# Kernel tuning notes

Measured on AMD Instinct MI355X. Metric: run time of the kernel, lower is better.

## Reference

```python
import jax, jax.numpy as jnp
import numpy as np

B, N = 4, 65536
NUM_GROUP, GROUP_SIZE = 512, 64
EMB = 60


def setup_inputs() -> dict:
    key = jax.random.key(0)
    ks = jax.random.split(key, 8)
    inp = {
        'xyz': jax.random.uniform(ks[0], (B, N, 3), jnp.float32),
        'color': jax.random.uniform(ks[1], (B, N, 3), jnp.float32),
        'W1': jax.random.normal(ks[2], (6, 64), jnp.float32) * 0.2,
        'b1': jnp.zeros((64,), jnp.float32),
        'W2': jax.random.normal(ks[3], (64, 128), jnp.float32) * 0.1,
        'b2': jnp.zeros((128,), jnp.float32),
        'W3': jax.random.normal(ks[4], (128, 256), jnp.float32) * 0.08,
        'b3': jnp.zeros((256,), jnp.float32),
        'W4': jax.random.normal(ks[5], (256, 512), jnp.float32) * 0.06,
        'b4': jnp.zeros((512,), jnp.float32),
        'Wp': jax.random.normal(ks[6], (512, EMB), jnp.float32) * 0.04,
        'bp': jnp.zeros((EMB,), jnp.float32),
    }
    return inp


def fps(xyz, n):
    """Farthest point sampling. xyz: (B,N,3) -> centers (B,n,3)."""
    b, npts, _ = xyz.shape
    start = jnp.zeros((b,), jnp.int32)
    d0 = jnp.full((b, npts), 1e10, xyz.dtype)

    def step(carry, _):
        dists, last = carry
        p = jnp.take_along_axis(xyz, last[:, None, None], axis=1)  # (B,1,3)
        d = jnp.sum((xyz - p) ** 2, axis=-1)                       # (B,N)
        dists = jnp.minimum(dists, d)
        nxt = jnp.argmax(dists, axis=-1).astype(jnp.int32)
        return (dists, nxt), nxt

    (_, _), rest = jax.lax.scan(step, (d0, start), None, length=n - 1)
    idx = jnp.concatenate([start[:, None], rest.T], axis=1)        # (B,n)
    return jax.vmap(lambda pts, i: pts[i])(xyz, idx)


def knn_idx(k, xyz, new_xyz):
    """Indices of k nearest points in xyz for each query in new_xyz.
    xyz: (B,N,3), new_xyz: (B,S,3) -> (B,S,k) int32. Matches
    square_distance + topk(largest=False)."""
    sq = (jnp.sum(new_xyz ** 2, -1)[..., None]
          + jnp.sum(xyz ** 2, -1)[:, None, :]
          - 2.0 * jnp.einsum('bsc,bnc->bsn', new_xyz, xyz))        # (B,S,N)
    _, idx = jax.lax.top_k(-sq, k)
    return idx


def reference(xyz, color, W1, b1, W2, b2, W3, b3, W4, b4, Wp, bp):
    # --- Group: FPS centers + KNN neighborhood gather + centering ---
    center = fps(xyz, NUM_GROUP)                                   # (B,G,3)
    idx = knn_idx(GROUP_SIZE, xyz, center)                         # (B,G,M)
    gather = jax.vmap(lambda pts, i: pts[i])                       # pts[(B,)N,3], i (G,M)
    neighborhood = gather(xyz, idx) - center[:, :, None, :]        # (B,G,M,3) centered
    neighborhood_color = gather(color, idx)                        # (B,G,M,3)
    feats = jnp.concatenate([neighborhood, neighborhood_color], -1)  # (B,G,M,6)

    # --- PointNet: per-point MLP -> max over group -> projection ---
    x = jax.nn.relu(feats @ W1 + b1)
    x = jax.nn.relu(x @ W2 + b2)
    x = jax.nn.relu(x @ W3 + b3)
    x = jax.nn.relu(x @ W4 + b4)                                   # (B,G,M,512)
    x = jnp.max(x, axis=2)                                         # (B,G,512)
    emb = x @ Wp + bp                                              # (B,G,60)
    return emb, center
```

## Files before the change

### kernel.cpp

```cpp
#include <hip/hip_runtime.h>
#include <stdint.h>

#define DI __device__ __forceinline__

typedef _Float16 f16x8 __attribute__((ext_vector_type(8)));
typedef float f32x4 __attribute__((ext_vector_type(4)));

constexpr int kB = 4;
constexpr int kN = 65536;
constexpr int kG = 512;
constexpr int kM = 64;
constexpr int kE = 60;
constexpr int GRD = 20;
constexpr int NCELL = GRD * GRD * GRD;
constexpr float CW = 1.0f / 20.0f;

constexpr int FPS_SUB = 8;
constexpr int FPS_PT_T = kN / FPS_SUB / 1024;

constexpr size_t OFF_WIN    = 0;
constexpr size_t OFF_CNT    = OFF_WIN + (size_t)kB * kG * 8;
constexpr size_t OFF_CCNT   = OFF_CNT + (size_t)kB * kG * 4;
constexpr size_t ZERO_BYTES = OFF_CCNT + (size_t)kB * NCELL * 4;
constexpr size_t OFF_CSTART = ZERO_BYTES;
constexpr size_t OFF_CUR    = OFF_CSTART + (size_t)kB * (NCELL + 1) * 4;
constexpr size_t OFF_SW1    = ((OFF_CUR + (size_t)kB * NCELL * 4) + 255) & ~(size_t)255;
constexpr size_t OFF_SW2    = OFF_SW1 + 2048 * 2;
constexpr size_t OFF_SW3    = OFF_SW2 + 8192 * 2;
constexpr size_t OFF_SW4    = OFF_SW3 + 32768 * 2;
constexpr size_t OFF_WPT    = OFF_SW4 + 131072 * 2;
constexpr size_t OFF_SORT   = ((OFF_WPT + 60 * 512 * 4) + 255) & ~(size_t)255;
constexpr size_t OFF_KIDX   = OFF_SORT + (size_t)kB * kN * 16;

DI int cellof(float x) {
  int c = (int)(x * (float)GRD);
  return min(GRD - 1, max(0, c));
}
DI unsigned orderable(float f) {
  unsigned u = __float_as_uint(f);
  return (u & 0x80000000u) ? ~u : (u | 0x80000000u);
}

__global__ void k_zero(uint32_t* p, int nwords) {
  int i = blockIdx.x * blockDim.x + threadIdx.x;
  int st = gridDim.x * blockDim.x;
  for (; i < nwords; i += st) p[i] = 0u;
}

DI void swz(const float* __restrict__ W, _Float16* __restrict__ sw,
            int total, int nks, int Kreal, int N, int i0, int st) {
  for (int i = i0; i < total; i += st) {
    int j = i & 7, lane = (i >> 3) & 63, rest = i >> 9;
    int ks = rest % nks, nt = rest / nks;
    int k = ks * 32 + ((lane >> 4) << 3) + j;
    int n = nt * 16 + (lane & 15);
    sw[i] = (_Float16)((k < Kreal) ? W[k * N + n] : 0.f);
  }
}

__global__ void k_prep(const float* __restrict__ W1, const float* __restrict__ W2,
                       const float* __restrict__ W3, const float* __restrict__ W4,
                       const float* __restrict__ Wp,
                       _Float16* __restrict__ sw1, _Float16* __restrict__ sw2,
                       _Float16* __restrict__ sw3, _Float16* __restrict__ sw4,
                       float* __restrict__ wpt) {
  int i0 = blockIdx.x * blockDim.x + threadIdx.x;
  int st = gridDim.x * blockDim.x;
  swz(W1, sw1, 2048, 1, 6, 64, i0, st);
  swz(W2, sw2, 8192, 2, 64, 128, i0, st);
  swz(W3, sw3, 32768, 4, 128, 256, i0, st);
  swz(W4, sw4, 131072, 8, 256, 512, i0, st);
  for (int i = i0; i < 60 * 512; i += st) { int n = i >> 9, k = i & 511; wpt[i] = Wp[k * 60 + n]; }
}

__global__ __launch_bounds__(1024) void k_fps(const float* __restrict__ xyz,
                                              float* __restrict__ outC,
                                              unsigned long long* __restrict__ win,
                                              unsigned int* __restrict__ cnt) {
  const int b = blockIdx.x >> 3, sub = blockIdx.x & 7;
  const int tid = threadIdx.x;
  const float* X = xyz + (size_t)b * kN * 3;
  float px[FPS_PT_T], py[FPS_PT_T], pz[FPS_PT_T], dd[FPS_PT_T];
#pragma unroll
  for (int j = 0; j < FPS_PT_T; ++j) {
    int p = sub * (kN / FPS_SUB) + j * 1024 + tid;
    px[j] = X[3 * p]; py[j] = X[3 * p + 1]; pz[j] = X[3 * p + 2];
    dd[j] = 1e10f;
  }
  float lx = X[0], ly = X[1], lz = X[2];
  if (sub == 0 && tid == 0) {
    outC[(size_t)b * kG * 3 + 0] = lx;
    outC[(size_t)b * kG * 3 + 1] = ly;
    outC[(size_t)b * kG * 3 + 2] = lz;
  }
  __shared__ unsigned long long wres[16];
  __shared__ float sp[3];
  unsigned long long* winB = win + (size_t)b * kG;
  unsigned int* cntB = cnt + (size_t)b * kG;

  for (int it = 1; it < kG; ++it) {
    unsigned long long best = 0ull;
#pragma unroll
    for (int j = 0; j < FPS_PT_T; ++j) {
      float dx = __fsub_rn(px[j], lx);
      float dy = __fsub_rn(py[j], ly);
      float dz = __fsub_rn(pz[j], lz);
      float d = __fadd_rn(__fadd_rn(__fmul_rn(dx, dx), __fmul_rn(dy, dy)), __fmul_rn(dz, dz));
      float nd = fminf(dd[j], d);
      dd[j] = nd;
      int p = sub * (kN / FPS_SUB) + j * 1024 + tid;
      unsigned long long pk =
          ((unsigned long long)__float_as_uint(nd) << 32) | (unsigned)(0xFFFFFFFFu - (unsigned)p);
      best = (pk > best) ? pk : best;
    }
#pragma unroll
    for (int off = 32; off; off >>= 1) {
      unsigned long long o = __shfl_down(best, (unsigned)off);
      best = (o > best) ? o : best;
    }
    if ((tid & 63) == 0) wres[tid >> 6] = best;
    __syncthreads();
    if (tid == 0) {
      unsigned long long bb = wres[0];
#pragma unroll
      for (int i = 1; i < 16; ++i) bb = (wres[i] > bb) ? wres[i] : bb;
      atomicMax(winB + it, bb | (1ull << 63));
      __threadfence();
      atomicAdd(cntB + it, 1u);
      long bail = 0;
      while (__hip_atomic_load(cntB + it, __ATOMIC_ACQUIRE, __HIP_MEMORY_SCOPE_AGENT) < (unsigned)FPS_SUB) {
        __builtin_amdgcn_s_sleep(1);
        if (++bail > 100000000L) break;
      }
      unsigned long long w = __hip_atomic_load(winB + it, __ATOMIC_ACQUIRE, __HIP_MEMORY_SCOPE_AGENT);
      int wi = (int)(0xFFFFFFFFu - (unsigned)(w & 0xFFFFFFFFu));
      float wx = X[3 * wi], wy = X[3 * wi + 1], wz = X[3 * wi + 2];
      sp[0] = wx; sp[1] = wy; sp[2] = wz;
      if (sub == 0) {
        outC[((size_t)b * kG + it) * 3 + 0] = wx;
        outC[((size_t)b * kG + it) * 3 + 1] = wy;
        outC[((size_t)b * kG + it) * 3 + 2] = wz;
      }
    }
    __syncthreads();
    lx = sp[0]; ly = sp[1]; lz = sp[2];
  }
}

__global__ void k_cellcount(const float* __restrict__ xyz, uint32_t* __restrict__ ccnt) {
  int i = blockIdx.x * blockDim.x + threadIdx.x;
  int st = gridDim.x * blockDim.x;
  for (; i < kB * kN; i += st) {
    int b = i >> 16, p = i & (kN - 1);
    const float* q = xyz + ((size_t)b * kN + p) * 3;
    int cid = (cellof(q[2]) * GRD + cellof(q[1])) * GRD + cellof(q[0]);
    atomicAdd(&ccnt[b * NCELL + cid], 1u);
  }
}

__global__ void k_scan(const uint32_t* __restrict__ ccnt, uint32_t* __restrict__ cstart,
                       uint32_t* __restrict__ cur) {
  int b = blockIdx.x, tid = threadIdx.x;
  const uint32_t* cc = ccnt + (size_t)b * NCELL;
  uint32_t* cs = cstart + (size_t)b * (NCELL + 1);
  uint32_t* cu = cur + (size_t)b * NCELL;
  __shared__ uint32_t part[256];
  const int chunk = 32;
  int c0 = tid * chunk;
  uint32_t s = 0;
  for (int i = 0; i < chunk; ++i) { int c = c0 + i; if (c < NCELL) s += cc[c]; }
  part[tid] = s;
  __syncthreads();
  for (int off = 1; off < 256; off <<= 1) {
    uint32_t add = (tid >= off) ? part[tid - off] : 0u;
    __syncthreads();
    part[tid] += add;
    __syncthreads();
  }
  uint32_t run = part[tid] - s;
  for (int i = 0; i < chunk; ++i) {
    int c = c0 + i;
    if (c < NCELL) { cs[c] = run; cu[c] = run; run += cc[c]; }
  }
  if (tid == 255) cs[NCELL] = run;
}

__global__ void k_scatter(const float* __restrict__ xyz, uint32_t* __restrict__ cur,
                          float4* __restrict__ sorted) {
  int i = blockIdx.x * blockDim.x + threadIdx.x;
  int st = gridDim.x * blockDim.x;
  for (; i < kB * kN; i += st) {
    int b = i >> 16, p = i & (kN - 1);
    const float* q = xyz + ((size_t)b * kN + p) * 3;
    float x = q[0], y = q[1], z = q[2];
    int cid = (cellof(z) * GRD + cellof(y)) * GRD + cellof(x);
    uint32_t pos = atomicAdd(&cur[b * NCELL + cid], 1u);
    sorted[(size_t)b * kN + pos] = make_float4(x, y, z, __uint_as_float((unsigned)p));
  }
}

constexpr int CAP = 8192;

DI void bitonic(unsigned long long* a, int n, int tid) {
  for (int k = 2; k <= n; k <<= 1)
    for (int j = k >> 1; j > 0; j >>= 1) {
      __syncthreads();
      for (int i = tid; i < n; i += 256) {
        int ix = i ^ j;
        if (ix > i) {
          unsigned long long x = a[i], y = a[ix];
          bool up = ((i & k) == 0);
          if ((x > y) == up) { a[i] = y; a[ix] = x; }
        }
      }
    }
  __syncthreads();
}

__global__ __launch_bounds__(256) void k_knn(const float4* __restrict__ sorted,
                                             const uint32_t* __restrict__ cstart,
                                             const float* __restrict__ outC,
                                             uint32_t* __restrict__ kidx) {
  const int bi = blockIdx.x;
  const int b = (bi & 7) >> 1;
  const int g = ((bi >> 3) << 1) | (bi & 1);
  const int tid = threadIdx.x;
  __shared__ unsigned long long cand[CAP];
  __shared__ int nC;
  const float cx = outC[((size_t)b * kG + g) * 3 + 0];
  const float cy = outC[((size_t)b * kG + g) * 3 + 1];
  const float cz = outC[((size_t)b * kG + g) * 3 + 2];
  const float nc = __fadd_rn(__fadd_rn(__fmul_rn(cx, cx), __fmul_rn(cy, cy)), __fmul_rn(cz, cz));
  const float4* SP = sorted + (size_t)b * kN;
  const uint32_t* CS = cstart + (size_t)b * (NCELL + 1);
  const int ccx = cellof(cx), ccy = cellof(cy), ccz = cellof(cz);
  if (tid == 0) nC = 0;
  __syncthreads();
  int plox = 1, phix = 0, ploy = 1, phiy = 0, ploz = 1, phiz = 0;
  for (int r = 1; r <= GRD; ++r) {
    int lox = max(0, ccx - r), hix = min(GRD - 1, ccx + r);
    int loy = max(0, ccy - r), hiy = min(GRD - 1, ccy + r);
    int loz = max(0, ccz - r), hiz = min(GRD - 1, ccz + r);
    for (int z = loz; z <= hiz; ++z)
      for (int y = loy; y <= hiy; ++y) {
        bool rowPrev = (r > 1) && (z >= ploz && z <= phiz && y >= ploy && y <= phiy);
        for (int s = 0; s < 2; ++s) {
          int xa, xb;
          if (!rowPrev) { if (s) break; xa = lox; xb = hix; }
          else if (s == 0) { xa = lox; xb = plox - 1; }
          else { xa = phix + 1; xb = hix; }
          if (xa > xb) continue;
          int c0 = (z * GRD + y) * GRD + xa;
          int i0 = CS[c0];
          int i1 = CS[(z * GRD + y) * GRD + xb + 1];
          for (int i = i0 + tid; i < i1; i += 256) {
            float4 pt = SP[i];
            float npn = __fadd_rn(__fadd_rn(__fmul_rn(pt.x, pt.x), __fmul_rn(pt.y, pt.y)),
                                  __fmul_rn(pt.z, pt.z));
            float dot = __fadd_rn(__fadd_rn(__fmul_rn(cx, pt.x), __fmul_rn(cy, pt.y)),
                                  __fmul_rn(cz, pt.z));
            float sq = __fsub_rn(__fadd_rn(nc, npn), __fmul_rn(2.0f, dot));
            unsigned key = orderable(sq);
            int pos = atomicAdd(&nC, 1);
            if (pos < CAP)
              cand[pos] = ((unsigned long long)key << 32) | (unsigned)__float_as_uint(pt.w);
          }
        }
      }
    __syncthreads();
    int n = min(nC, CAP);
    float rc = 1e30f;
    if (lox > 0) rc = fminf(rc, cx - (float)lox * CW);
    if (hix < GRD - 1) rc = fminf(rc, (float)(hix + 1) * CW - cx);
    if (loy > 0) rc = fminf(rc, cy - (float)loy * CW);
    if (hiy < GRD - 1) rc = fminf(rc, (float)(hiy + 1) * CW - cy);
    if (loz > 0) rc = fminf(rc, cz - (float)loz * CW);
    if (hiz < GRD - 1) rc = fminf(rc, (float)(hiz + 1) * CW - cz);
    float r2 = (rc >= 1e29f) ? 3.0e38f : rc * rc * (1.0f - 1e-5f);
    unsigned keyR = orderable(r2);
    bool done = false;
    if (n >= kM) {
      int np2 = 1;
      while (np2 < n) np2 <<= 1;
      for (int i = n + tid; i < np2; i += 256) cand[i] = ~0ull;
      bitonic(cand, np2, tid);
      unsigned k63 = (unsigned)(cand[kM - 1] >> 32);
      done = (k63 <= keyR);
      if (tid == 0) nC = n;
    }
    __syncthreads();
    if (done) break;
    plox = lox; phix = hix; ploy = loy; phiy = hiy; ploz = loz; phiz = hiz;
  }
  if (tid < kM)
    kidx[((size_t)b * kG + g) * kM + tid] = (uint32_t)(cand[tid] & 0xFFFFFFFFu);
}


template <int Kdim, int Ndim, int SIN, int SOUT>
DI void mfma_layer(const _Float16* __restrict__ Xin, _Float16* __restrict__ Xout,
                   const _Float16* __restrict__ Wsw, const float* __restrict__ bias,
                   int wave, int lane) {
  constexpr int NKS = Kdim / 32;
  constexpr int NTW = Ndim / 64;
  constexpr int CH = (NTW < 4) ? NTW : 4;
  const int quad = lane >> 4, l16 = lane & 15;
  for (int c0 = 0; c0 < NTW; c0 += CH) {
    f32x4 acc[CH][4];
#pragma unroll
    for (int nt = 0; nt < CH; ++nt) {
      float bv = bias[wave * (Ndim / 4) + (c0 + nt) * 16 + l16];
#pragma unroll
      for (int m = 0; m < 4; ++m) acc[nt][m] = {bv, bv, bv, bv};
    }
#pragma unroll
    for (int ks = 0; ks < NKS; ++ks) {
      f16x8 af[4];
#pragma unroll
      for (int m = 0; m < 4; ++m)
        af[m] = *(const f16x8*)(Xin + (m * 16 + l16) * SIN + ks * 32 + quad * 8);
#pragma unroll
      for (int nt = 0; nt < CH; ++nt) {
        int ntg = wave * NTW + c0 + nt;
        f16x8 bf = *(const f16x8*)(Wsw + ((size_t)(ntg * NKS + ks) * 64 + lane) * 8);
#pragma unroll
        for (int m = 0; m < 4; ++m)
          acc[nt][m] = __builtin_amdgcn_mfma_f32_16x16x32_f16(af[m], bf, acc[nt][m], 0, 0, 0);
      }
    }
#pragma unroll
    for (int nt = 0; nt < CH; ++nt) {
      int col = wave * (Ndim / 4) + (c0 + nt) * 16 + l16;
#pragma unroll
      for (int m = 0; m < 4; ++m)
#pragma unroll
        for (int r = 0; r < 4; ++r) {
          int row = m * 16 + quad * 4 + r;
          Xout[row * SOUT + col] = (_Float16)fmaxf(acc[nt][m][r], 0.f);
        }
    }
  }
}

DI void mfma_layer4(const _Float16* __restrict__ Xin, const _Float16* __restrict__ Wsw,
                    const float* __restrict__ bias, float* __restrict__ maxv,
                    int wave, int lane) {
  constexpr int SIN = 264, NKS = 8, NTW = 8, CH = 4;
  const int quad = lane >> 4, l16 = lane & 15;
  for (int c0 = 0; c0 < NTW; c0 += CH) {
    f32x4 acc[CH][4];
#pragma unroll
    for (int nt = 0; nt < CH; ++nt) {
      float bv = bias[wave * 128 + (c0 + nt) * 16 + l16];
#pragma unroll
      for (int m = 0; m < 4; ++m) acc[nt][m] = {bv, bv, bv, bv};
    }
#pragma unroll
    for (int ks = 0; ks < NKS; ++ks) {
      f16x8 af[4];
#pragma unroll
      for (int m = 0; m < 4; ++m)
        af[m] = *(const f16x8*)(Xin + (m * 16 + l16) * SIN + ks * 32 + quad * 8);
#pragma unroll
      for (int nt = 0; nt < CH; ++nt) {
        int ntg = wave * NTW + c0 + nt;
        f16x8 bf = *(const f16x8*)(Wsw + ((size_t)(ntg * NKS + ks) * 64 + lane) * 8);
#pragma unroll
        for (int m = 0; m < 4; ++m)
          acc[nt][m] = __builtin_amdgcn_mfma_f32_16x16x32_f16(af[m], bf, acc[nt][m], 0, 0, 0);
      }
    }
#pragma unroll
    for (int nt = 0; nt < CH; ++nt) {
      float mx = 0.f;
#pragma unroll
      for (int m = 0; m < 4; ++m)
#pragma unroll
        for (int r = 0; r < 4; ++r) mx = fmaxf(mx, acc[nt][m][r]);
      mx = fmaxf(mx, __shfl_xor(mx, 16, 64));
      mx = fmaxf(mx, __shfl_xor(mx, 32, 64));
      if (quad == 0) maxv[wave * 128 + (c0 + nt) * 16 + l16] = mx;
    }
  }
}

__global__ __launch_bounds__(256) void k_mlp(
    const float* __restrict__ xyz, const float* __restrict__ color,
    const float* __restrict__ outC, const uint32_t* __restrict__ kidx,
    const _Float16* __restrict__ sw1, const _Float16* __restrict__ sw2,
    const _Float16* __restrict__ sw3, const _Float16* __restrict__ sw4,
    const float* __restrict__ wpt,
    const float* __restrict__ b1, const float* __restrict__ b2,
    const float* __restrict__ b3, const float* __restrict__ b4,
    const float* __restrict__ bp, float* __restrict__ outE) {
  const int bi = blockIdx.x;
  const int b = (bi & 7) >> 1;
  const int g = ((bi >> 3) << 1) | (bi & 1);
  const int tid = threadIdx.x;
  const int wave = tid >> 6, lane = tid & 63;
  __shared__ __align__(16) char smem[17408 + 33792];
  _Float16* bufA = (_Float16*)smem;
  _Float16* bufB = (_Float16*)(smem + 17408);
  float* maxv = (float*)smem;
  float* psum = (float*)(smem + 2048);

  if (tid < kM) {
    uint32_t p = kidx[((size_t)b * kG + g) * kM + tid];
    const float* cen = outC + ((size_t)b * kG + g) * 3;
    const float* xp = xyz + ((size_t)b * kN + p) * 3;
    const float* cp = color + ((size_t)b * kN + p) * 3;
    f16x8 v = {};
    v[0] = (_Float16)__fsub_rn(xp[0], cen[0]);
    v[1] = (_Float16)__fsub_rn(xp[1], cen[1]);
    v[2] = (_Float16)__fsub_rn(xp[2], cen[2]);
    v[3] = (_Float16)cp[0];
    v[4] = (_Float16)cp[1];
    v[5] = (_Float16)cp[2];
    f16x8 z = {};
    *(f16x8*)(bufA + tid * 40 + 0) = v;
    *(f16x8*)(bufA + tid * 40 + 8) = z;
    *(f16x8*)(bufA + tid * 40 + 16) = z;
    *(f16x8*)(bufA + tid * 40 + 24) = z;
  }
  __syncthreads();
  mfma_layer<32, 64, 40, 72>(bufA, bufB, sw1, b1, wave, lane);
  __syncthreads();
  mfma_layer<64, 128, 72, 136>(bufB, bufA, sw2, b2, wave, lane);
  __syncthreads();
  mfma_layer<128, 256, 136, 264>(bufA, bufB, sw3, b3, wave, lane);
  __syncthreads();
  mfma_layer4(bufB, sw4, b4, maxv, wave, lane);
  __syncthreads();
  if (tid < 240) {
    int j = tid >> 2, q = tid & 3;
    const float* w = wpt + (size_t)j * 512 + q * 128;
    float s = 0.f;
#pragma unroll 4
    for (int k = 0; k < 128; ++k) s = fmaf(maxv[q * 128 + k], w[k], s);
    psum[tid] = s;
  }
  __syncthreads();
  if (tid < kE) {
    float e = __fadd_rn(__fadd_rn(psum[tid * 4 + 0], psum[tid * 4 + 1]),
                        __fadd_rn(psum[tid * 4 + 2], psum[tid * 4 + 3])) + bp[tid];
    outE[((size_t)b * kG + g) * kE + tid] = e;
  }
}

extern "C" void kernel_launch(void* const* d_in, const int* in_sizes, int n_in,
                              void* d_out, int out_size, void* d_ws, size_t ws_size,
                              hipStream_t stream) {
  (void)in_sizes; (void)n_in; (void)out_size; (void)ws_size;
  const float* xyz = (const float*)d_in[0];
  const float* color = (const float*)d_in[1];
  const float* W1 = (const float*)d_in[2];
  const float* b1 = (const float*)d_in[3];
  const float* W2 = (const float*)d_in[4];
  const float* b2 = (const float*)d_in[5];
  const float* W3 = (const float*)d_in[6];
  const float* b3 = (const float*)d_in[7];
  const float* W4 = (const float*)d_in[8];
  const float* b4 = (const float*)d_in[9];
  const float* Wp = (const float*)d_in[10];
  const float* bp = (const float*)d_in[11];

  char* ws = (char*)d_ws;
  auto win = (unsigned long long*)(ws + OFF_WIN);
  auto cnt = (unsigned int*)(ws + OFF_CNT);
  auto ccnt = (uint32_t*)(ws + OFF_CCNT);
  auto cstart = (uint32_t*)(ws + OFF_CSTART);
  auto cur = (uint32_t*)(ws + OFF_CUR);
  auto sw1 = (_Float16*)(ws + OFF_SW1);
  auto sw2 = (_Float16*)(ws + OFF_SW2);
  auto sw3 = (_Float16*)(ws + OFF_SW3);
  auto sw4 = (_Float16*)(ws + OFF_SW4);
  auto wpt = (float*)(ws + OFF_WPT);
  auto sorted = (float4*)(ws + OFF_SORT);
  auto kidx = (uint32_t*)(ws + OFF_KIDX);

  float* outE = (float*)d_out;
  float* outC = outE + (size_t)kB * kG * kE;

  k_zero<<<64, 256, 0, stream>>>((uint32_t*)ws, (int)(ZERO_BYTES / 4));
  k_prep<<<256, 256, 0, stream>>>(W1, W2, W3, W4, Wp, sw1, sw2, sw3, sw4, wpt);
  k_fps<<<kB * FPS_SUB, 1024, 0, stream>>>(xyz, outC, win, cnt);
  k_cellcount<<<512, 256, 0, stream>>>(xyz, ccnt);
  k_scan<<<kB, 256, 0, stream>>>(ccnt, cstart, cur);
  k_scatter<<<512, 256, 0, stream>>>(xyz, cur, sorted);
  k_knn<<<kB * kG, 256, 0, stream>>>(sorted, cstart, outC, kidx);
  k_mlp<<<kB * kG, 256, 0, stream>>>(xyz, color, outC, kidx, sw1, sw2, sw3, sw4, wpt,
                                     b1, b2, b3, b4, bp, outE);
}
```

Measured before the change: 2.001 ms.

## Replace FPS atomicMax+counter barrier with per-block slot publish and wave-wide poll

Each FPS block now publishes its local winner key and coordinates into its own slot with a release store. One wave then polls all eight slots in parallel and reduces them locally. This removes the serialized atomicMax, fence and counter round-trip, as well as the dependent global load of the winning point's coordinates. The packed key keeps only 16 bits of index, relying on the per-block point range fitting in 16 bits. The zeroed workspace grows to hold the per-iteration slots.

```diff
diff --git a/kernel.cpp b/kernel.cpp
--- a/kernel.cpp
+++ b/kernel.cpp
@@ -19,8 +19,7 @@
 constexpr int FPS_PT_T = kN / FPS_SUB / 1024;
 
 constexpr size_t OFF_WIN    = 0;
-constexpr size_t OFF_CNT    = OFF_WIN + (size_t)kB * kG * 8;
-constexpr size_t OFF_CCNT   = OFF_CNT + (size_t)kB * kG * 4;
+constexpr size_t OFF_CCNT   = OFF_WIN + (size_t)kB * kG * 256;
 constexpr size_t ZERO_BYTES = OFF_CCNT + (size_t)kB * NCELL * 4;
 constexpr size_t OFF_CSTART = ZERO_BYTES;
 constexpr size_t OFF_CUR    = OFF_CSTART + (size_t)kB * (NCELL + 1) * 4;
@@ -73,12 +72,20 @@
   for (int i = i0; i < 60 * 512; i += st) { int n = i >> 9, k = i & 511; wpt[i] = Wp[k * 60 + n]; }
 }
 
+DI void redstep(unsigned long long& k, float& x, float& y, float& z, int off) {
+  unsigned long long ok = __shfl_down(k, off);
+  float ox = __shfl_down(x, off);
+  float oy = __shfl_down(y, off);
+  float oz = __shfl_down(z, off);
+  if (ok > k) { k = ok; x = ox; y = oy; z = oz; }
+}
+
 __global__ __launch_bounds__(1024) void k_fps(const float* __restrict__ xyz,
                                               float* __restrict__ outC,
-                                              unsigned long long* __restrict__ win,
-                                              unsigned int* __restrict__ cnt) {
+                                              unsigned long long* __restrict__ win) {
   const int b = blockIdx.x >> 3, sub = blockIdx.x & 7;
   const int tid = threadIdx.x;
+  const int wave = tid >> 6, lane = tid & 63;
   const float* X = xyz + (size_t)b * kN * 3;
   float px[FPS_PT_T], py[FPS_PT_T], pz[FPS_PT_T], dd[FPS_PT_T];
 #pragma unroll
@@ -93,13 +100,14 @@
     outC[(size_t)b * kG * 3 + 1] = ly;
     outC[(size_t)b * kG * 3 + 2] = lz;
   }
-  __shared__ unsigned long long wres[16];
+  __shared__ unsigned long long wkey[16];
+  __shared__ float wx[16], wy[16], wz[16];
   __shared__ float sp[3];
-  unsigned long long* winB = win + (size_t)b * kG;
-  unsigned int* cntB = cnt + (size_t)b * kG;
+  unsigned long long* winB = win + (size_t)b * kG * 32;
 
   for (int it = 1; it < kG; ++it) {
-    unsigned long long best = 0ull;
+    unsigned long long bk = 0ull;
+    float bx = 0.f, by = 0.f, bz = 0.f;
 #pragma unroll
     for (int j = 0; j < FPS_PT_T; ++j) {
       float dx = __fsub_rn(px[j], lx);
@@ -109,37 +117,58 @@
       float nd = fminf(dd[j], d);
       dd[j] = nd;
       int p = sub * (kN / FPS_SUB) + j * 1024 + tid;
-      unsigned long long pk =
-          ((unsigned long long)__float_as_uint(nd) << 32) | (unsigned)(0xFFFFFFFFu - (unsigned)p);
-      best = (pk > best) ? pk : best;
-    }
-#pragma unroll
-    for (int off = 32; off; off >>= 1) {
-      unsigned long long o = __shfl_down(best, (unsigned)off);
-      best = (o > best) ? o : best;
-    }
-    if ((tid & 63) == 0) wres[tid >> 6] = best;
+      unsigned long long pk = (1ull << 63) | ((unsigned long long)__float_as_uint(nd) << 16) |
+                              (unsigned long long)(0xFFFFu - (unsigned)p);
+      if (pk > bk) { bk = pk; bx = px[j]; by = py[j]; bz = pz[j]; }
+    }
+#pragma unroll
+    for (int off = 32; off; off >>= 1) redstep(bk, bx, by, bz, off);
+    if (lane == 0) { wkey[wave] = bk; wx[wave] = bx; wy[wave] = by; wz[wave] = bz; }
     __syncthreads();
-    if (tid == 0) {
-      unsigned long long bb = wres[0];
-#pragma unroll
-      for (int i = 1; i < 16; ++i) bb = (wres[i] > bb) ? wres[i] : bb;
-      atomicMax(winB + it, bb | (1ull << 63));
-      __threadfence();
-      atomicAdd(cntB + it, 1u);
+    if (wave == 0) {
+      unsigned long long k2 = (lane < 16) ? wkey[lane] : 0ull;
+      float x2 = (lane < 16) ? wx[lane] : 0.f;
+      float y2 = (lane < 16) ? wy[lane] : 0.f;
+      float z2 = (lane < 16) ? wz[lane] : 0.f;
+      redstep(k2, x2, y2, z2, 8);
+      redstep(k2, x2, y2, z2, 4);
+      redstep(k2, x2, y2, z2, 2);
+      redstep(k2, x2, y2, z2, 1);
+      unsigned long long* base = winB + (size_t)it * 32;
+      if (lane == 0) {
+        unsigned long long xyv = ((unsigned long long)__float_as_uint(x2) << 32) |
+                                 (unsigned long long)__float_as_uint(y2);
+        __hip_atomic_store(base + 8 + sub, xyv, __ATOMIC_RELAXED, __HIP_MEMORY_SCOPE_AGENT);
+        __hip_atomic_store(base + 16 + sub, (unsigned long long)__float_as_uint(z2),
+                           __ATOMIC_RELAXED, __HIP_MEMORY_SCOPE_AGENT);
+        __hip_atomic_store(base + sub, k2, __ATOMIC_RELEASE, __HIP_MEMORY_SCOPE_AGENT);
+      }
+      int s = lane & 7;
+      unsigned long long kk;
       long bail = 0;
-      while (__hip_atomic_load(cntB + it, __ATOMIC_ACQUIRE, __HIP_MEMORY_SCOPE_AGENT) < (unsigned)FPS_SUB) {
-        __builtin_amdgcn_s_sleep(1);
+      for (;;) {
+        kk = __hip_atomic_load(base + s, __ATOMIC_ACQUIRE, __HIP_MEMORY_SCOPE_AGENT);
+        unsigned long long rdy = __ballot(kk >> 63);
+        if (rdy == ~0ull) break;
         if (++bail > 100000000L) break;
       }
-      unsigned long long w = __hip_atomic_load(winB + it, __ATOMIC_ACQUIRE, __HIP_MEMORY_SCOPE_AGENT);
-      int wi = (int)(0xFFFFFFFFu - (unsigned)(w & 0xFFFFFFFFu));
-      float wx = X[3 * wi], wy = X[3 * wi + 1], wz = X[3 * wi + 2];
-      sp[0] = wx; sp[1] = wy; sp[2] = wz;
-      if (sub == 0) {
-        outC[((size_t)b * kG + it) * 3 + 0] = wx;
-        outC[((size_t)b * kG + it) * 3 + 1] = wy;
-        outC[((size_t)b * kG + it) * 3 + 2] = wz;
+      unsigned long long xyv = __hip_atomic_load(base + 8 + s, __ATOMIC_RELAXED,
+                                                 __HIP_MEMORY_SCOPE_AGENT);
+      unsigned long long zv = __hip_atomic_load(base + 16 + s, __ATOMIC_RELAXED,
+                                                __HIP_MEMORY_SCOPE_AGENT);
+      float fx = __uint_as_float((unsigned)(xyv >> 32));
+      float fy = __uint_as_float((unsigned)(xyv & 0xFFFFFFFFu));
+      float fz = __uint_as_float((unsigned)(zv & 0xFFFFFFFFu));
+      redstep(kk, fx, fy, fz, 4);
+      redstep(kk, fx, fy, fz, 2);
+      redstep(kk, fx, fy, fz, 1);
+      if (lane == 0) {
+        sp[0] = fx; sp[1] = fy; sp[2] = fz;
+        if (sub == 0) {
+          outC[((size_t)b * kG + it) * 3 + 0] = fx;
+          outC[((size_t)b * kG + it) * 3 + 1] = fy;
+          outC[((size_t)b * kG + it) * 3 + 2] = fz;
+        }
       }
     }
     __syncthreads();
@@ -296,7 +325,6 @@
     kidx[((size_t)b * kG + g) * kM + tid] = (uint32_t)(cand[tid] & 0xFFFFFFFFu);
 }
 
-
 template <int Kdim, int Ndim, int SIN, int SOUT>
 DI void mfma_layer(const _Float16* __restrict__ Xin, _Float16* __restrict__ Xout,
                    const _Float16* __restrict__ Wsw, const float* __restrict__ bias,
@@ -466,7 +494,6 @@
 
   char* ws = (char*)d_ws;
   auto win = (unsigned long long*)(ws + OFF_WIN);
-  auto cnt = (unsigned int*)(ws + OFF_CNT);
   auto ccnt = (uint32_t*)(ws + OFF_CCNT);
   auto cstart = (uint32_t*)(ws + OFF_CSTART);
   auto cur = (uint32_t*)(ws + OFF_CUR);
@@ -481,9 +508,9 @@
   float* outE = (float*)d_out;
   float* outC = outE + (size_t)kB * kG * kE;
 
-  k_zero<<<64, 256, 0, stream>>>((uint32_t*)ws, (int)(ZERO_BYTES / 4));
+  k_zero<<<128, 256, 0, stream>>>((uint32_t*)ws, (int)(ZERO_BYTES / 4));
   k_prep<<<256, 256, 0, stream>>>(W1, W2, W3, W4, Wp, sw1, sw2, sw3, sw4, wpt);
-  k_fps<<<kB * FPS_SUB, 1024, 0, stream>>>(xyz, outC, win, cnt);
+  k_fps<<<kB * FPS_SUB, 1024, 0, stream>>>(xyz, outC, win);
   k_cellcount<<<512, 256, 0, stream>>>(xyz, ccnt);
   k_scan<<<kB, 256, 0, stream>>>(ccnt, cstart, cur);
   k_scatter<<<512, 256, 0, stream>>>(xyz, cur, sorted);
```

Result: slower. 2.379 ms (+18.9%).
